# Performance work log

Hardware: AMD Instinct MI355X
Metric: run time of the kernel (lower is better)

The kernel has to match this reference:

```python
import jax, jax.numpy as jnp
import numpy as np

BITS = 8192      # num_neurons / output bits per step
NB_T = 10        # n_bits_per_neuron for transition RAM (min(bits+4,10))
NB_I = 4         # n_bits_per_neuron for initial RAM
POS = 4          # position encoding bits
LENGTH = 4096


def setup_inputs() -> dict:
    key = jax.random.key(0)
    k1, k2, k3, k4 = jax.random.split(key, 4)
    # RAM contents are binary (0/1) stored as float32 for the kernel baseline
    transition_memory = (jax.random.uniform(k1, (BITS, 2 ** NB_T)) > 0.5).astype(jnp.float32)
    initial_memory = (jax.random.uniform(k2, (BITS, 2 ** NB_I)) > 0.5).astype(jnp.float32)
    # each neuron taps NB random bit positions of its input
    transition_connections = jax.random.randint(k3, (BITS, NB_T), 0, BITS + POS, dtype=jnp.int32)
    initial_connections = jax.random.randint(k4, (BITS, NB_I), 0, POS, dtype=jnp.int32)
    return {
        "transition_memory": transition_memory,
        "initial_memory": initial_memory,
        "transition_connections": transition_connections,
        "initial_connections": initial_connections,
        "length": LENGTH,
    }


def _pos_bits(pos):
    # matches _encode_pos: bits[3] = LSB, bits[0] = MSB of low 4 bits
    return ((pos >> jnp.arange(3, -1, -1, dtype=jnp.int32)) & 1).astype(jnp.int32)


def _ram(x_bits, connections, memory):
    # x_bits: [total_input_bits] int32 in {0,1}
    sel = x_bits[connections]                                  # [N, n]
    n = connections.shape[1]
    pw = (2 ** jnp.arange(n - 1, -1, -1)).astype(jnp.int32)    # bit -> address weight
    addr = (sel * pw).sum(-1)                                  # [N]
    return jnp.take_along_axis(memory, addr[:, None], axis=1)[:, 0]  # [N]


def reference(transition_memory, initial_memory, transition_connections, initial_connections, length):
    # step 0: initial RAM addressed by position bits only
    out0 = _ram(_pos_bits(jnp.int32(0)), initial_connections, initial_memory)  # [BITS] float {0,1}

    def step(prev_bits, i):
        inp = jnp.concatenate([prev_bits, _pos_bits(i)])                      # [BITS+4]
        out = _ram(inp, transition_connections, transition_memory)            # [BITS]
        return (out > 0.5).astype(jnp.int32), out

    _, outs = jax.lax.scan(step, (out0 > 0.5).astype(jnp.int32),
                           jnp.arange(1, length, dtype=jnp.int32))
    return jnp.concatenate([out0[None, :], outs], axis=0)  # [length, BITS]
```

## Files before the change

### kernel.cpp

```cpp
#include <hip/hip_runtime.h>
#include <stdint.h>


#define BITS   8192
#define NBT    10
#define NBLK   16
#define TPB    512
#define NPB    (BITS / NBLK)
#define SWORDS 256
#define WPB    (NPB / 32)
#define FUSE   (1 << 12)

__global__ void pack_kernel(const float* __restrict__ tm, uint32_t* __restrict__ packed) {
    int tid = blockIdx.x * blockDim.x + threadIdx.x;
    float v = tm[tid];
    unsigned long long m = __ballot(v > 0.5f);
    int lane = tid & 63;
    if ((lane & 31) == 0) {
        packed[tid >> 5] = (lane == 0) ? (uint32_t)m : (uint32_t)(m >> 32);
    }
}

__global__ __launch_bounds__(TPB) void ram_step_kernel(
    const int* __restrict__ conn,
    const float* __restrict__ init_mem,
    const uint32_t* __restrict__ packedT,
    unsigned long long* __restrict__ pairs,
    float* __restrict__ out,
    int length)
{
    const int b = blockIdx.x;
    const int t = threadIdx.x;
    const int lane = t & 63;
    const int n = b * NPB + t;

    __shared__ uint32_t st[SWORDS + 1];

    int c[NBT];
#pragma unroll
    for (int j = 0; j < NBT; ++j) c[j] = conn[n * NBT + j];

    float v0 = init_mem[n << 4];
    out[n] = v0;
    int bit = (v0 > 0.5f) ? 1 : 0;
    unsigned long long m = __ballot(bit);
    const int gw = b * WPB + (t >> 6) * 2;
    if (lane == 0) {
        const unsigned long long tag = 1ull << 32;
        __hip_atomic_store(&pairs[gw],     tag | (uint32_t)m,
                           __ATOMIC_RELAXED, __HIP_MEMORY_SCOPE_AGENT);
        __hip_atomic_store(&pairs[gw + 1], tag | (uint32_t)(m >> 32),
                           __ATOMIC_RELAXED, __HIP_MEMORY_SCOPE_AGENT);
        st[gw]     = (uint32_t)m;
        st[gw + 1] = (uint32_t)(m >> 32);
    }

    for (int i = 1; i < length; ++i) {
        const int parity = (i - 1) & 1;
        const uint32_t want = (uint32_t)i;

        if (t == 0) {
            st[SWORDS] = ((i >> 3) & 1) | (((i >> 2) & 1) << 1) |
                         (((i >> 1) & 1) << 2) | ((i & 1) << 3);
        }
        if (t < SWORDS && (t >> 4) != b) {
            unsigned long long* p = &pairs[parity * SWORDS + t];
            unsigned long long pv;
            int fuse = 0;
            do {
                pv = __hip_atomic_load(p, __ATOMIC_RELAXED, __HIP_MEMORY_SCOPE_AGENT);
            } while ((uint32_t)(pv >> 32) != want && ++fuse < FUSE);
            st[t] = (uint32_t)pv;
        }
        __syncthreads();

        uint32_t addr = 0;
#pragma unroll
        for (int j = 0; j < NBT; ++j) {
            int cc = c[j];
            uint32_t w = st[cc >> 5];
            addr = (addr << 1) | ((w >> (cc & 31)) & 1u);
        }
        uint32_t pw = packedT[(n << 5) + (addr >> 5)];
        bit = (pw >> (addr & 31)) & 1;
        out[(size_t)i * BITS + n] = (float)bit;

        m = __ballot(bit);
        if (lane == 0) {
            const unsigned long long tag = ((unsigned long long)(i + 1)) << 32;
            const int base = (i & 1) * SWORDS + gw;
            __hip_atomic_store(&pairs[base],     tag | (uint32_t)m,
                               __ATOMIC_RELAXED, __HIP_MEMORY_SCOPE_AGENT);
            __hip_atomic_store(&pairs[base + 1], tag | (uint32_t)(m >> 32),
                               __ATOMIC_RELAXED, __HIP_MEMORY_SCOPE_AGENT);
        }
        __syncthreads();
        if (lane == 0) {
            st[gw]     = (uint32_t)m;
            st[gw + 1] = (uint32_t)(m >> 32);
        }
    }
}

extern "C" void kernel_launch(void* const* d_in, const int* in_sizes, int n_in,
                              void* d_out, int out_size, void* d_ws, size_t ws_size,
                              hipStream_t stream) {
    const float* tm = (const float*)d_in[0];
    const float* im = (const float*)d_in[1];
    const int*   tc = (const int*)d_in[2];
    const int length = out_size / BITS;

    uint32_t* packed = (uint32_t*)d_ws;
    unsigned long long* pairs =
        (unsigned long long*)((char*)d_ws + (1 << 20));

    hipMemsetAsync(pairs, 0, 2 * SWORDS * sizeof(unsigned long long), stream);

    pack_kernel<<<dim3((BITS * 1024) / 256), dim3(256), 0, stream>>>(tm, packed);

    ram_step_kernel<<<dim3(NBLK), dim3(TPB), 0, stream>>>(
        tc, im, packed, pairs, (float*)d_out, length);
}
```

Before: 5.810 ms.

## Cache per-block transition table in LDS and double-buffer state words

Spreads the neurons over 32 blocks of 256 threads. Each block preloads its slice of the packed transition table into shared memory, so the per-step RAM lookup reads LDS instead of global memory. The shared state buffer is double-buffered, which removes the second barrier per step, and the output store now happens after the ballot publish so other blocks see the new bits sooner. The trade-off is more blocks taking part in the cross-block spin-wait each step, which adds polling traffic and more places for the step to be delayed.

```diff
diff --git a/kernel.cpp b/kernel.cpp
--- a/kernel.cpp
+++ b/kernel.cpp
@@ -4,11 +4,12 @@
 
 #define BITS   8192
 #define NBT    10
-#define NBLK   16
-#define TPB    512
+#define NBLK   32
+#define TPB    256
 #define NPB    (BITS / NBLK)
 #define SWORDS 256
 #define WPB    (NPB / 32)
+#define TWORDS (NPB * 32)
 #define FUSE   (1 << 12)
 
 __global__ void pack_kernel(const float* __restrict__ tm, uint32_t* __restrict__ packed) {
@@ -34,43 +35,55 @@
     const int lane = t & 63;
     const int n = b * NPB + t;
 
-    __shared__ uint32_t st[SWORDS + 1];
+    __shared__ uint32_t st[2][SWORDS + 1];
+    __shared__ uint32_t tbl[TWORDS];
+
+    {
+        const uint32_t* tp = packedT + (size_t)b * TWORDS;
+#pragma unroll
+        for (int k = 0; k < 8; ++k) {
+            int w = k * 1024 + t * 4;
+            uint4 v = *(const uint4*)(tp + w);
+            *(uint4*)&tbl[w] = v;
+        }
+    }
 
     int c[NBT];
 #pragma unroll
     for (int j = 0; j < NBT; ++j) c[j] = conn[n * NBT + j];
 
+    const int gw = b * WPB + (t >> 6) * 2;
+
     float v0 = init_mem[n << 4];
-    out[n] = v0;
     int bit = (v0 > 0.5f) ? 1 : 0;
     unsigned long long m = __ballot(bit);
-    const int gw = b * WPB + (t >> 6) * 2;
     if (lane == 0) {
         const unsigned long long tag = 1ull << 32;
         __hip_atomic_store(&pairs[gw],     tag | (uint32_t)m,
                            __ATOMIC_RELAXED, __HIP_MEMORY_SCOPE_AGENT);
         __hip_atomic_store(&pairs[gw + 1], tag | (uint32_t)(m >> 32),
                            __ATOMIC_RELAXED, __HIP_MEMORY_SCOPE_AGENT);
-        st[gw]     = (uint32_t)m;
-        st[gw + 1] = (uint32_t)(m >> 32);
+        st[0][gw]     = (uint32_t)m;
+        st[0][gw + 1] = (uint32_t)(m >> 32);
     }
+    out[n] = v0;
 
     for (int i = 1; i < length; ++i) {
-        const int parity = (i - 1) & 1;
+        uint32_t* sb = st[(i - 1) & 1];
         const uint32_t want = (uint32_t)i;
 
         if (t == 0) {
-            st[SWORDS] = ((i >> 3) & 1) | (((i >> 2) & 1) << 1) |
+            sb[SWORDS] = ((i >> 3) & 1) | (((i >> 2) & 1) << 1) |
                          (((i >> 1) & 1) << 2) | ((i & 1) << 3);
         }
-        if (t < SWORDS && (t >> 4) != b) {
-            unsigned long long* p = &pairs[parity * SWORDS + t];
+        if ((t >> 3) != b) {
+            unsigned long long* p = &pairs[((i - 1) & 1) * SWORDS + t];
             unsigned long long pv;
             int fuse = 0;
             do {
                 pv = __hip_atomic_load(p, __ATOMIC_RELAXED, __HIP_MEMORY_SCOPE_AGENT);
             } while ((uint32_t)(pv >> 32) != want && ++fuse < FUSE);
-            st[t] = (uint32_t)pv;
+            sb[t] = (uint32_t)pv;
         }
         __syncthreads();
 
@@ -78,12 +91,10 @@
 #pragma unroll
         for (int j = 0; j < NBT; ++j) {
             int cc = c[j];
-            uint32_t w = st[cc >> 5];
-            addr = (addr << 1) | ((w >> (cc & 31)) & 1u);
+            addr = (addr << 1) | ((sb[cc >> 5] >> (cc & 31)) & 1u);
         }
-        uint32_t pw = packedT[(n << 5) + (addr >> 5)];
+        uint32_t pw = tbl[(t << 5) + (addr >> 5)];
         bit = (pw >> (addr & 31)) & 1;
-        out[(size_t)i * BITS + n] = (float)bit;
 
         m = __ballot(bit);
         if (lane == 0) {
@@ -93,12 +104,10 @@
                                __ATOMIC_RELAXED, __HIP_MEMORY_SCOPE_AGENT);
             __hip_atomic_store(&pairs[base + 1], tag | (uint32_t)(m >> 32),
                                __ATOMIC_RELAXED, __HIP_MEMORY_SCOPE_AGENT);
+            st[i & 1][gw]     = (uint32_t)m;
+            st[i & 1][gw + 1] = (uint32_t)(m >> 32);
         }
-        __syncthreads();
-        if (lane == 0) {
-            st[gw]     = (uint32_t)m;
-            st[gw + 1] = (uint32_t)(m >> 32);
-        }
+        out[(size_t)i * BITS + n] = (float)bit;
     }
 }
 
```

Result: slower. 6.202 ms (+6.7%).

## Add dedicated poller wavefront with batched cache-bypassing loads for cross-block exchange

Applied to the files above, without the earlier changes.

Adds an extra 64-thread wavefront per block that only polls the other blocks' published bit-words. Each poller lane issues four sc0 sc1 global loads per round, so one wave covers all 240 remote words instead of 240 separate spinning threads. The compute waves now publish their own words to shared memory at the top of each step, leaving one barrier pair per step. The poller writes a sentinel value on timeout instead of stale data. The aim is lower per-step latency for the inter-block handshake, at the cost of a larger block and a barrier count that must match between the two roles.

```diff
diff --git a/kernel.cpp b/kernel.cpp
--- a/kernel.cpp
+++ b/kernel.cpp
@@ -5,11 +5,11 @@
 #define BITS   8192
 #define NBT    10
 #define NBLK   16
-#define TPB    512
-#define NPB    (BITS / NBLK)
+#define NPB    512
+#define TPB    (NPB + 64)
 #define SWORDS 256
-#define WPB    (NPB / 32)
-#define FUSE   (1 << 12)
+#define WPB    16
+#define BFUSE  1024
 
 __global__ void pack_kernel(const float* __restrict__ tm, uint32_t* __restrict__ packed) {
     int tid = blockIdx.x * blockDim.x + threadIdx.x;
@@ -32,72 +32,115 @@
     const int b = blockIdx.x;
     const int t = threadIdx.x;
     const int lane = t & 63;
-    const int n = b * NPB + t;
 
     __shared__ uint32_t st[SWORDS + 1];
 
-    int c[NBT];
+    if (t < NPB) {
+        const int n = b * NPB + t;
+        int c[NBT];
 #pragma unroll
-    for (int j = 0; j < NBT; ++j) c[j] = conn[n * NBT + j];
+        for (int j = 0; j < NBT; ++j) c[j] = conn[n * NBT + j];
 
-    float v0 = init_mem[n << 4];
-    out[n] = v0;
-    int bit = (v0 > 0.5f) ? 1 : 0;
-    unsigned long long m = __ballot(bit);
-    const int gw = b * WPB + (t >> 6) * 2;
-    if (lane == 0) {
-        const unsigned long long tag = 1ull << 32;
-        __hip_atomic_store(&pairs[gw],     tag | (uint32_t)m,
-                           __ATOMIC_RELAXED, __HIP_MEMORY_SCOPE_AGENT);
-        __hip_atomic_store(&pairs[gw + 1], tag | (uint32_t)(m >> 32),
-                           __ATOMIC_RELAXED, __HIP_MEMORY_SCOPE_AGENT);
-        st[gw]     = (uint32_t)m;
-        st[gw + 1] = (uint32_t)(m >> 32);
-    }
+        const int gw = b * WPB + (t >> 6) * 2;
 
-    for (int i = 1; i < length; ++i) {
-        const int parity = (i - 1) & 1;
-        const uint32_t want = (uint32_t)i;
-
-        if (t == 0) {
-            st[SWORDS] = ((i >> 3) & 1) | (((i >> 2) & 1) << 1) |
-                         (((i >> 1) & 1) << 2) | ((i & 1) << 3);
-        }
-        if (t < SWORDS && (t >> 4) != b) {
-            unsigned long long* p = &pairs[parity * SWORDS + t];
-            unsigned long long pv;
-            int fuse = 0;
-            do {
-                pv = __hip_atomic_load(p, __ATOMIC_RELAXED, __HIP_MEMORY_SCOPE_AGENT);
-            } while ((uint32_t)(pv >> 32) != want && ++fuse < FUSE);
-            st[t] = (uint32_t)pv;
-        }
-        __syncthreads();
-
-        uint32_t addr = 0;
-#pragma unroll
-        for (int j = 0; j < NBT; ++j) {
-            int cc = c[j];
-            uint32_t w = st[cc >> 5];
-            addr = (addr << 1) | ((w >> (cc & 31)) & 1u);
-        }
-        uint32_t pw = packedT[(n << 5) + (addr >> 5)];
-        bit = (pw >> (addr & 31)) & 1;
-        out[(size_t)i * BITS + n] = (float)bit;
-
-        m = __ballot(bit);
+        float v0 = init_mem[n << 4];
+        int bit = (v0 > 0.5f) ? 1 : 0;
+        unsigned long long m = __ballot(bit);
         if (lane == 0) {
-            const unsigned long long tag = ((unsigned long long)(i + 1)) << 32;
-            const int base = (i & 1) * SWORDS + gw;
-            __hip_atomic_store(&pairs[base],     tag | (uint32_t)m,
+            const unsigned long long tag = 1ull << 32;
+            __hip_atomic_store(&pairs[gw],     tag | (uint32_t)m,
                                __ATOMIC_RELAXED, __HIP_MEMORY_SCOPE_AGENT);
-            __hip_atomic_store(&pairs[base + 1], tag | (uint32_t)(m >> 32),
+            __hip_atomic_store(&pairs[gw + 1], tag | (uint32_t)(m >> 32),
                                __ATOMIC_RELAXED, __HIP_MEMORY_SCOPE_AGENT);
         }
-        __syncthreads();
-        if (lane == 0) {
-            st[gw]     = (uint32_t)m;
-            st[gw + 1] = (uint32_t)(m >> 32);
+        out[n] = v0;
+
+        for (int i = 1; i < length; ++i) {
+            if (lane == 0) {
+                st[gw]     = (uint32_t)m;
+                st[gw + 1] = (uint32_t)(m >> 32);
+            }
+            __syncthreads();
+
+            uint32_t addr = 0;
+#pragma unroll
+            for (int j = 0; j < NBT; ++j) {
+                int cc = c[j];
+                addr = (addr << 1) | ((st[cc >> 5] >> (cc & 31)) & 1u);
+            }
+            uint32_t pw = packedT[(n << 5) + (addr >> 5)];
+            bit = (pw >> (addr & 31)) & 1;
+            out[(size_t)i * BITS + n] = (float)bit;
+
+            m = __ballot(bit);
+            if (lane == 0) {
+                const unsigned long long tag = ((unsigned long long)(i + 1)) << 32;
+                const int base = (i & 1) * SWORDS + gw;
+                __hip_atomic_store(&pairs[base],     tag | (uint32_t)m,
+                                   __ATOMIC_RELAXED, __HIP_MEMORY_SCOPE_AGENT);
+                __hip_atomic_store(&pairs[base + 1], tag | (uint32_t)(m >> 32),
+                                   __ATOMIC_RELAXED, __HIP_MEMORY_SCOPE_AGENT);
+            }
+            __syncthreads();
+        }
+    } else {
+        const int l = t - NPB;
+        const bool have = (l < 60);
+        uint32_t w0 = 0, w1 = 0, w2 = 0, w3 = 0;
+        if (have) {
+            int r = l * 4;
+            w0 = r + 0 + ((r + 0) >= b * WPB ? WPB : 0);
+            w1 = r + 1 + ((r + 1) >= b * WPB ? WPB : 0);
+            w2 = r + 2 + ((r + 2) >= b * WPB ? WPB : 0);
+            w3 = r + 3 + ((r + 3) >= b * WPB ? WPB : 0);
+        }
+
+        for (int i = 1; i < length; ++i) {
+            if (l == 63) {
+                st[SWORDS] = ((i >> 3) & 1) | (((i >> 2) & 1) << 1) |
+                             (((i >> 1) & 1) << 2) | ((i & 1) << 3);
+            }
+            if (have) {
+                unsigned long long* base = &pairs[((i - 1) & 1) * SWORDS];
+                unsigned long long* a0 = base + w0;
+                unsigned long long* a1 = base + w1;
+                unsigned long long* a2 = base + w2;
+                unsigned long long* a3 = base + w3;
+                const uint32_t want = (uint32_t)i;
+                int need = 0xF;
+                for (int f = 0; f < BFUSE && need; ++f) {
+                    uint64_t v0, v1, v2, v3;
+                    asm volatile(
+                        "global_load_dwordx2 %0, %4, off sc0 sc1\n\t"
+                        "global_load_dwordx2 %1, %5, off sc0 sc1\n\t"
+                        "global_load_dwordx2 %2, %6, off sc0 sc1\n\t"
+                        "global_load_dwordx2 %3, %7, off sc0 sc1\n\t"
+                        "s_waitcnt vmcnt(0)"
+                        : "=&v"(v0), "=&v"(v1), "=&v"(v2), "=&v"(v3)
+                        : "v"(a0), "v"(a1), "v"(a2), "v"(a3)
+                        : "memory");
+                    if ((need & 1) && (uint32_t)(v0 >> 32) == want) {
+                        st[w0] = (uint32_t)v0; need &= ~1;
+                    }
+                    if ((need & 2) && (uint32_t)(v1 >> 32) == want) {
+                        st[w1] = (uint32_t)v1; need &= ~2;
+                    }
+                    if ((need & 4) && (uint32_t)(v2 >> 32) == want) {
+                        st[w2] = (uint32_t)v2; need &= ~4;
+                    }
+                    if ((need & 8) && (uint32_t)(v3 >> 32) == want) {
+                        st[w3] = (uint32_t)v3; need &= ~8;
+                    }
+                }
+                if (need) {
+                    if (need & 1) st[w0] = 0xDEADBEEFu;
+                    if (need & 2) st[w1] = 0xDEADBEEFu;
+                    if (need & 4) st[w2] = 0xDEADBEEFu;
+                    if (need & 8) st[w3] = 0xDEADBEEFu;
+                }
+            }
+            __syncthreads();
+            __syncthreads();
         }
     }
 }
```

Measured after the change: 8.569 ms. 47.5% more time.

## Poll peer state via global_load_lds with XOR-tagged words instead of atomic loads

Applied to the files above, without the earlier changes.

Replaces the per-word relaxed atomic polling loop with a 16-byte global-to-LDS async load (global_load_lds) per pair of words, validated by an XOR-hashed tag embedded in each 64-bit word. Each block now also reads its own words back through global memory, and every thread in a wavefront shares one LDS landing area. The intent is to cut the latency of cross-block step synchronization and the number of polling transactions. If the fast path ever fails, it falls back to the old atomic polling. The change leans on a raw s_waitcnt asm and on LDS-DMA semantics, so it risks memory-ordering mistakes and torn reads.

```diff
diff --git a/kernel.cpp b/kernel.cpp
--- a/kernel.cpp
+++ b/kernel.cpp
@@ -9,23 +9,33 @@
 #define NPB    (BITS / NBLK)
 #define SWORDS 256
 #define WPB    (NPB / 32)
-#define FUSE   (1 << 12)
+#define NPAIR  128
+#define KMUL   2654435761u
+#define AFUSE  (1 << 12)
+#define BFUSE  (1 << 14)
 
-__global__ void pack_kernel(const float* __restrict__ tm, uint32_t* __restrict__ packed) {
+typedef unsigned long long u64;
+typedef uint32_t u32;
+
+__global__ void pack_kernel(const float* __restrict__ tm, u32* __restrict__ packed) {
     int tid = blockIdx.x * blockDim.x + threadIdx.x;
     float v = tm[tid];
-    unsigned long long m = __ballot(v > 0.5f);
+    u64 m = __ballot(v > 0.5f);
     int lane = tid & 63;
     if ((lane & 31) == 0) {
-        packed[tid >> 5] = (lane == 0) ? (uint32_t)m : (uint32_t)(m >> 32);
+        packed[tid >> 5] = (lane == 0) ? (u32)m : (u32)(m >> 32);
     }
+}
+
+__device__ __forceinline__ u64 mkword(u32 lo, u32 tag) {
+    return ((u64)(tag ^ lo) << 32) | lo;
 }
 
 __global__ __launch_bounds__(TPB) void ram_step_kernel(
     const int* __restrict__ conn,
     const float* __restrict__ init_mem,
-    const uint32_t* __restrict__ packedT,
-    unsigned long long* __restrict__ pairs,
+    const u32* __restrict__ packedT,
+    u64* __restrict__ pairs,
     float* __restrict__ out,
     int length)
 {
@@ -34,7 +44,11 @@
     const int lane = t & 63;
     const int n = b * NPB + t;
 
-    __shared__ uint32_t st[SWORDS + 1];
+    __shared__ u32 st[SWORDS + 1];
+    __shared__ volatile u32 scr[2][NPAIR][4];
+    __shared__ int s_bad;
+
+    if (t == 0) s_bad = 0;
 
     int c[NBT];
 #pragma unroll
@@ -43,62 +57,85 @@
     float v0 = init_mem[n << 4];
     out[n] = v0;
     int bit = (v0 > 0.5f) ? 1 : 0;
-    unsigned long long m = __ballot(bit);
+    u64 m = __ballot(bit);
     const int gw = b * WPB + (t >> 6) * 2;
+    const int gp = gw >> 1;
     if (lane == 0) {
-        const unsigned long long tag = 1ull << 32;
-        __hip_atomic_store(&pairs[gw],     tag | (uint32_t)m,
+        __hip_atomic_store(&pairs[gp * 2],     mkword((u32)m, 1u * KMUL),
                            __ATOMIC_RELAXED, __HIP_MEMORY_SCOPE_AGENT);
-        __hip_atomic_store(&pairs[gw + 1], tag | (uint32_t)(m >> 32),
+        __hip_atomic_store(&pairs[gp * 2 + 1], mkword((u32)(m >> 32), 1u * KMUL),
                            __ATOMIC_RELAXED, __HIP_MEMORY_SCOPE_AGENT);
-        st[gw]     = (uint32_t)m;
-        st[gw + 1] = (uint32_t)(m >> 32);
     }
+    __syncthreads();
 
     for (int i = 1; i < length; ++i) {
-        const int parity = (i - 1) & 1;
-        const uint32_t want = (uint32_t)i;
+        const int par = (i - 1) & 1;
+        const u32 want = (u32)i * KMUL;
 
         if (t == 0) {
             st[SWORDS] = ((i >> 3) & 1) | (((i >> 2) & 1) << 1) |
                          (((i >> 1) & 1) << 2) | ((i & 1) << 3);
         }
-        if (t < SWORDS && (t >> 4) != b) {
-            unsigned long long* p = &pairs[parity * SWORDS + t];
-            unsigned long long pv;
-            int fuse = 0;
-            do {
-                pv = __hip_atomic_load(p, __ATOMIC_RELAXED, __HIP_MEMORY_SCOPE_AGENT);
-            } while ((uint32_t)(pv >> 32) != want && ++fuse < FUSE);
-            st[t] = (uint32_t)pv;
+        if (t < NPAIR) {
+            const u32* gsrc = (const u32*)&pairs[(par * NPAIR + t) * 2];
+            volatile u32* lbase = &scr[par][(t >> 6) << 6][0];
+            bool done = false;
+            u32 d0 = 0xDEADBEEFu, d1 = 0xDEADBEEFu;
+            if (!s_bad) {
+                for (int f = 0; f < AFUSE && !done; ++f) {
+                    __builtin_amdgcn_global_load_lds(
+                        (const __attribute__((address_space(1))) u32*)gsrc,
+                        (__attribute__((address_space(3))) u32*)lbase,
+                        16, 0, 17 );
+                    asm volatile("s_waitcnt vmcnt(8)" ::: "memory");
+                    u32 a0 = scr[par][t][0], a1 = scr[par][t][1];
+                    u32 a2 = scr[par][t][2], a3 = scr[par][t][3];
+                    if (((a0 ^ a1) == want) && ((a2 ^ a3) == want)) {
+                        d0 = a0; d1 = a2; done = true;
+                    }
+                }
+                if (!done) s_bad = 1;
+            }
+            if (!done) {
+                const u64* q = &pairs[(par * NPAIR + t) * 2];
+                u64 w0, w1;
+                int f = 0;
+                do { w0 = __hip_atomic_load(q, __ATOMIC_RELAXED,
+                                            __HIP_MEMORY_SCOPE_AGENT);
+                } while ((((u32)(w0 >> 32)) ^ (u32)w0) != want && ++f < BFUSE);
+                f = 0;
+                do { w1 = __hip_atomic_load(q + 1, __ATOMIC_RELAXED,
+                                            __HIP_MEMORY_SCOPE_AGENT);
+                } while ((((u32)(w1 >> 32)) ^ (u32)w1) != want && ++f < BFUSE);
+                if ((((u32)(w0 >> 32)) ^ (u32)w0) == want) d0 = (u32)w0;
+                if ((((u32)(w1 >> 32)) ^ (u32)w1) == want) d1 = (u32)w1;
+            }
+            st[2 * t]     = d0;
+            st[2 * t + 1] = d1;
         }
         __syncthreads();
 
-        uint32_t addr = 0;
+        u32 addr = 0;
 #pragma unroll
         for (int j = 0; j < NBT; ++j) {
             int cc = c[j];
-            uint32_t w = st[cc >> 5];
+            u32 w = st[cc >> 5];
             addr = (addr << 1) | ((w >> (cc & 31)) & 1u);
         }
-        uint32_t pw = packedT[(n << 5) + (addr >> 5)];
+        u32 pw = packedT[(n << 5) + (addr >> 5)];
         bit = (pw >> (addr & 31)) & 1;
         out[(size_t)i * BITS + n] = (float)bit;
 
         m = __ballot(bit);
         if (lane == 0) {
-            const unsigned long long tag = ((unsigned long long)(i + 1)) << 32;
-            const int base = (i & 1) * SWORDS + gw;
-            __hip_atomic_store(&pairs[base],     tag | (uint32_t)m,
+            const u32 tg = (u32)(i + 1) * KMUL;
+            const int base = ((i & 1) * NPAIR + gp) * 2;
+            __hip_atomic_store(&pairs[base],     mkword((u32)m, tg),
                                __ATOMIC_RELAXED, __HIP_MEMORY_SCOPE_AGENT);
-            __hip_atomic_store(&pairs[base + 1], tag | (uint32_t)(m >> 32),
+            __hip_atomic_store(&pairs[base + 1], mkword((u32)(m >> 32), tg),
                                __ATOMIC_RELAXED, __HIP_MEMORY_SCOPE_AGENT);
         }
         __syncthreads();
-        if (lane == 0) {
-            st[gw]     = (uint32_t)m;
-            st[gw + 1] = (uint32_t)(m >> 32);
-        }
     }
 }
 
@@ -110,11 +147,10 @@
     const int*   tc = (const int*)d_in[2];
     const int length = out_size / BITS;
 
-    uint32_t* packed = (uint32_t*)d_ws;
-    unsigned long long* pairs =
-        (unsigned long long*)((char*)d_ws + (1 << 20));
+    u32* packed = (u32*)d_ws;
+    u64* pairs  = (u64*)((char*)d_ws + (1 << 20));
 
-    hipMemsetAsync(pairs, 0, 2 * SWORDS * sizeof(unsigned long long), stream);
+    hipMemsetAsync(pairs, 0, 2 * NPAIR * 2 * sizeof(u64), stream);
 
     pack_kernel<<<dim3((BITS * 1024) / 256), dim3(256), 0, stream>>>(tm, packed);
 
```

Result: slower. 6.893 ms (+18.6%).
